# Optimization experiments

Measured on AMD Instinct MI355X. Metric: run time of the kernel, lower is better.

The kernel has to match this reference:

```python
import jax, jax.numpy as jnp
import numpy as np

B, N, D, H, FF = 2, 2048, 768, 12, 3072
HD = D // H
RADIUS = 2.0
COORD_DIM = 3
LN_EPS = 1e-5


def _layernorm(x, g, b):
    m = jnp.mean(x, axis=-1, keepdims=True)
    v = jnp.mean((x - m) ** 2, axis=-1, keepdims=True)
    return (x - m) * jax.lax.rsqrt(v + LN_EPS) * g + b


def setup_inputs() -> dict:
    key = jax.random.key(0)
    ks = jax.random.split(key, 16)
    s = 0.02
    return {
        "x": jax.random.normal(ks[0], (B, N, D), jnp.float32),
        "coords": jax.random.uniform(ks[1], (B, N, COORD_DIM), jnp.float32) * 10.0,
        "w_qkv": jax.random.normal(ks[2], (D, 3 * D), jnp.float32) * s,
        "b_qkv": jnp.zeros((3 * D,), jnp.float32),
        "w_out": jax.random.normal(ks[3], (D, D), jnp.float32) * s,
        "b_out": jnp.zeros((D,), jnp.float32),
        "w_ff1": jax.random.normal(ks[4], (D, FF), jnp.float32) * s,
        "b_ff1": jnp.zeros((FF,), jnp.float32),
        "w_ff2": jax.random.normal(ks[5], (FF, D), jnp.float32) * s,
        "b_ff2": jnp.zeros((D,), jnp.float32),
        "g1": jnp.ones((D,), jnp.float32),
        "beta1": jnp.zeros((D,), jnp.float32),
        "g2": jnp.ones((D,), jnp.float32),
        "beta2": jnp.zeros((D,), jnp.float32),
    }


def reference(x, coords, w_qkv, b_qkv, w_out, b_out, w_ff1, b_ff1,
              w_ff2, b_ff2, g1, beta1, g2, beta2):
    # --- attention sub-block ---
    residual = x
    xn = _layernorm(x, g1, beta1)
    qkv = xn @ w_qkv + b_qkv                       # [B,N,3D]
    qkv = qkv.reshape(B, N, 3, H, HD)
    q, k, v = qkv[:, :, 0], qkv[:, :, 1], qkv[:, :, 2]   # [B,N,H,HD]

    # geometric radius mask: attend only to tokens within Euclidean RADIUS
    d2 = jnp.sum((coords[:, :, None, :] - coords[:, None, :, :]) ** 2, axis=-1)  # [B,N,N]
    mask = d2 <= RADIUS * RADIUS                   # self-distance 0 -> always true

    scores = jnp.einsum("bqhd,bkhd->bhqk", q, k) / jnp.sqrt(jnp.float32(HD))
    scores = jnp.where(mask[:, None, :, :], scores, jnp.float32(-1e9))
    attn = jax.nn.softmax(scores, axis=-1)
    attn_out = jnp.einsum("bhqk,bkhd->bqhd", attn, v).reshape(B, N, D)
    attn_out = attn_out @ w_out + b_out            # dropout=0 (eval)
    x = residual + attn_out

    # --- FFN sub-block ---
    residual = x
    xn = _layernorm(x, g2, beta2)
    h = jax.nn.gelu(xn @ w_ff1 + b_ff1, approximate=False)
    ff_out = h @ w_ff2 + b_ff2
    return residual + ff_out
```

## Files before the change

### kernel.cpp

```cpp
#include <hip/hip_runtime.h>
#include <hip/hip_bf16.h>

typedef unsigned short ushort_t;
typedef __attribute__((ext_vector_type(4))) float f32x4;
typedef __attribute__((ext_vector_type(8))) short s16x8;

#define DEV static __device__ __forceinline__

constexpr int Bb = 2, Nn = 2048, Dd = 768, Hh = 12, FFf = 3072;
constexpr int MTOK = Bb * Nn;
constexpr int QKVN = 3 * Dd;

DEV unsigned short f2bf(float f) {
    union { float f; unsigned int i; } x; x.f = f;
    unsigned int r = x.i + 0x7FFFu + ((x.i >> 16) & 1u);
    return (unsigned short)(r >> 16);
}

DEV void gload16(const void* g, void* l) {
    __builtin_amdgcn_global_load_lds(
        (const __attribute__((address_space(1))) void*)g,
        (__attribute__((address_space(3))) void*)l, 16, 0, 0);
}

DEV int xcd_swz(int lin, int n) {
    return (lin & 7) * (n >> 3) + (lin >> 3);
}

__global__ void k_transpose(const float* __restrict__ in, unsigned short* __restrict__ out,
                            int K, int N) {
    __shared__ float t[32][33];
    int bx = blockIdx.x * 32, by = blockIdx.y * 32;
    int tx = threadIdx.x, ty = threadIdx.y;
#pragma unroll
    for (int i = 0; i < 4; i++)
        t[ty + 8 * i][tx] = in[(size_t)(by + ty + 8 * i) * N + bx + tx];
    __syncthreads();
#pragma unroll
    for (int i = 0; i < 4; i++)
        out[(size_t)(bx + ty + 8 * i) * K + by + tx] = f2bf(t[tx][ty + 8 * i]);
}

__global__ void k_coords(const float* __restrict__ c, float4* __restrict__ out, int n) {
    int i = blockIdx.x * 256 + threadIdx.x;
    if (i < n) out[i] = make_float4(c[3 * i], c[3 * i + 1], c[3 * i + 2], 0.f);
}

DEV int cell_of(float4 c) {
    int cx = (int)(c.x * 0.5f); cx = cx > 4 ? 4 : cx;
    int cy = (int)(c.y * 0.5f); cy = cy > 4 ? 4 : cy;
    int cz = (int)(c.z * 0.5f); cz = cz > 4 ? 4 : cz;
    return (cz * 5 + cy) * 5 + cx;
}

__global__ __launch_bounds__(256) void k_sort(const float4* __restrict__ c4,
                                              int* __restrict__ s2o,
                                              float4* __restrict__ c4s) {
    int b = blockIdx.y;
    int i = blockIdx.x * 4 + (threadIdx.x >> 6);
    int lane = threadIdx.x & 63;
    const float4* cb = c4 + b * Nn;
    float4 ci = cb[i];
    int celli = cell_of(ci);
    int pos = 0;
    for (int it = 0; it < Nn / 64; it++) {
        int j = it * 64 + lane;
        int cj = cell_of(cb[j]);
        bool before = (cj < celli) || (cj == celli && j < i);
        pos += __popcll(__ballot(before));
    }
    if (lane == 0) {
        s2o[b * Nn + pos] = i;
        c4s[b * Nn + pos] = ci;
    }
}

__global__ __launch_bounds__(256) void k_mask(const float4* __restrict__ c4s,
                                              unsigned long long* __restrict__ mb) {
    int qt = blockIdx.x, ks = blockIdx.y, b = blockIdx.z;
    __shared__ float4 ck[256];
    int t = threadIdx.x;
    ck[t] = c4s[b * Nn + ks * 256 + t];
    __syncthreads();
    int r = t >> 2, c = t & 3;
    int q = qt * 64 + r;
    float4 cq = c4s[b * Nn + q];
    unsigned long long w = 0;
#pragma unroll 8
    for (int j = 0; j < 64; j++) {
        float4 k4 = ck[c * 64 + j];
        float dx = __fsub_rn(cq.x, k4.x);
        float dy = __fsub_rn(cq.y, k4.y);
        float dz = __fsub_rn(cq.z, k4.z);
        float d2 = __fadd_rn(__fadd_rn(__fmul_rn(dx, dx), __fmul_rn(dy, dy)),
                             __fmul_rn(dz, dz));
        if (d2 <= 4.0f) w |= 1ull << j;
    }
    mb[((size_t)(b * Nn + q) << 5) + ks * 4 + c] = w;
}

__global__ __launch_bounds__(64) void k_tiles(const unsigned long long* __restrict__ mb,
                                              int* __restrict__ tl) {
    int q64 = blockIdx.x, b = blockIdx.y;
    int lane = threadIdx.x;
    unsigned long long v = 0;
    if (lane < 32) {
        const unsigned long long* base = mb + ((size_t)(b * Nn + q64 * 64) << 5) + lane;
        for (int r = 0; r < 64; r++) v |= base[(size_t)r << 5];
    }
    unsigned long long nz = __ballot(v != 0);
    int idx = __popcll(nz & ((1ull << lane) - 1));
    int* o = tl + (b * 32 + q64) * 33;
    if (v != 0) o[1 + idx] = lane;
    if (lane == 0) o[0] = __popcll(nz);
}

__global__ __launch_bounds__(128) void k_gatherK(const unsigned short* __restrict__ qkv,
                                                 const int* __restrict__ s2o,
                                                 unsigned short* __restrict__ Ksort) {
    int ns = blockIdx.x & (Nn - 1);
    int b = blockIdx.x >> 11;
    int t = threadIdx.x;
    int orig = s2o[b * Nn + ns];
    const s16x8* src = (const s16x8*)(qkv + ((size_t)b * Nn + orig) * QKVN + Dd);
    s16x8* dst = (s16x8*)(Ksort + ((size_t)b * Nn + ns) * Dd);
    if (t < 96) dst[t] = src[t];
}

__global__ __launch_bounds__(256) void k_vt(const unsigned short* __restrict__ qkv,
                                            const int* __restrict__ s2o,
                                            unsigned short* __restrict__ VtT) {
    __shared__ unsigned short Ld[64][72];
    int ns0 = blockIdx.x * 64;
    int bh = blockIdx.y;
    int b = bh / Hh, h = bh % Hh;
    int t = threadIdx.x;
#pragma unroll
    for (int i = 0; i < 2; i++) {
        int item = t + 256 * i;
        int row = item >> 3, ch = (item & 7) * 8;
        int orig = s2o[b * Nn + ns0 + row];
        *(s16x8*)&Ld[row][ch] =
            *(const s16x8*)(qkv + ((size_t)b * Nn + orig) * QKVN + 2 * Dd + h * 64 + ch);
    }
    __syncthreads();
    int vd = (t >> 5) * 8, vkp = (t & 31) * 2;
#pragma unroll
    for (int j = 0; j < 8; j++) {
        unsigned int pack = (unsigned int)Ld[vkp][vd + j] |
                            ((unsigned int)Ld[vkp + 1][vd + j] << 16);
        *(unsigned int*)((char*)VtT +
                         (((size_t)bh * 64 + vd + j) * Nn + ns0 + vkp) * 2) = pack;
    }
}

DEV float wred_sum(float v) {
#pragma unroll
    for (int o = 32; o; o >>= 1) v += __shfl_down(v, o, 64);
    return v;
}

__global__ __launch_bounds__(256) void k_ln(const float* __restrict__ x,
                                            const float* __restrict__ g,
                                            const float* __restrict__ be,
                                            unsigned short* __restrict__ out) {
    int row = blockIdx.x;
    const float* xr = x + (size_t)row * Dd;
    int t = threadIdx.x;
    float v0 = xr[t], v1 = xr[t + 256], v2 = xr[t + 512];
    float s = v0 + v1 + v2;
    float sq = v0 * v0 + v1 * v1 + v2 * v2;
    __shared__ float r1[4], r2[4];
    float ws = wred_sum(s), wq = wred_sum(sq);
    int wid = t >> 6, lane = t & 63;
    if (lane == 0) { r1[wid] = ws; r2[wid] = wq; }
    __syncthreads();
    s = r1[0] + r1[1] + r1[2] + r1[3];
    sq = r2[0] + r2[1] + r2[2] + r2[3];
    float mean = s * (1.f / Dd);
    float var = sq * (1.f / Dd) - mean * mean;
    float rs = rsqrtf(var + 1e-5f);
    unsigned short* orow = out + (size_t)row * Dd;
    orow[t]       = f2bf((v0 - mean) * rs * g[t]       + be[t]);
    orow[t + 256] = f2bf((v1 - mean) * rs * g[t + 256] + be[t + 256]);
    orow[t + 512] = f2bf((v2 - mean) * rs * g[t + 512] + be[t + 512]);
}

template <int EPI>
__global__ __launch_bounds__(256) void k_gemm(const unsigned short* __restrict__ A,
                                              const unsigned short* __restrict__ Bt,
                                              const float* __restrict__ bias,
                                              const float* __restrict__ res,
                                              void* __restrict__ outp,
                                              int M, int N, int K) {
    constexpr int BM = 128, BN = 128, BK = 32;
    __shared__ unsigned short As[BM][BK];
    __shared__ unsigned short Bs[BN][BK];
    int NB = N >> 7;
    int id = xcd_swz(blockIdx.x, gridDim.x);
    int m0 = (id / NB) * BM, n0 = (id % NB) * BN;
    int t = threadIdx.x;
    int wid = t >> 6, lane = t & 63;
    int wr = wid >> 1, wc = wid & 1;
    int lg = lane >> 4, lr = lane & 15;
    f32x4 acc[4][4] = {};

    int srow = wid * 32 + (lane >> 2);
    int scol = (lane & 3) * 8;
    const unsigned short* Ag = A + (size_t)(m0 + srow) * K + scol;
    const unsigned short* Bg = Bt + (size_t)(n0 + srow) * K + scol;
    char* Al = (char*)&As[0][0] + wid * 2048;
    char* Bl = (char*)&Bs[0][0] + wid * 2048;

    for (int k0 = 0; k0 < K; k0 += BK) {
        __syncthreads();
        gload16(Ag + k0, Al);
        gload16(Ag + k0 + (size_t)16 * K, Al + 1024);
        gload16(Bg + k0, Bl);
        gload16(Bg + k0 + (size_t)16 * K, Bl + 1024);
        __syncthreads();
        s16x8 af[4], bfr[4];
#pragma unroll
        for (int i = 0; i < 4; i++) {
            af[i]  = *(const s16x8*)&As[wr * 64 + i * 16 + lr][lg * 8];
            bfr[i] = *(const s16x8*)&Bs[wc * 64 + i * 16 + lr][lg * 8];
        }
#pragma unroll
        for (int mi = 0; mi < 4; mi++)
#pragma unroll
            for (int ni = 0; ni < 4; ni++)
                acc[mi][ni] = __builtin_amdgcn_mfma_f32_16x16x32_bf16(
                    af[mi], bfr[ni], acc[mi][ni], 0, 0, 0);
    }

    int mrow = m0 + wr * 64;
    int ncol = n0 + wc * 64;
#pragma unroll
    for (int mi = 0; mi < 4; mi++) {
#pragma unroll
        for (int ni = 0; ni < 4; ni++) {
            int nn = ncol + ni * 16 + lr;
            float bs = bias[nn];
#pragma unroll
            for (int r = 0; r < 4; r++) {
                int mm = mrow + mi * 16 + lg * 4 + r;
                float v = acc[mi][ni][r] + bs;
                if (EPI == 1) {
                    v = 0.5f * v * (1.f + erff(v * 0.70710678118f));
                    ((unsigned short*)outp)[(size_t)mm * N + nn] = f2bf(v);
                } else if (EPI == 2) {
                    v += res[(size_t)mm * N + nn];
                    ((float*)outp)[(size_t)mm * N + nn] = v;
                } else {
                    ((unsigned short*)outp)[(size_t)mm * N + nn] = f2bf(v);
                }
            }
        }
    }
}

template <int SPLIT>
__global__ __launch_bounds__(256) void k_gemm_sk(const unsigned short* __restrict__ A,
                                                 const unsigned short* __restrict__ Bt,
                                                 float* __restrict__ part,
                                                 int M, int N, int K) {
    constexpr int BM = 128, BN = 128, BK = 32;
    __shared__ unsigned short As[BM][BK];
    __shared__ unsigned short Bs[BN][BK];
    int NB = N >> 7, MB = M >> 7;
    int id = xcd_swz(blockIdx.x, gridDim.x);
    int nb = id % NB;
    int mb = (id / NB) % MB;
    int kz = id / (NB * MB);
    int m0 = mb * BM, n0 = nb * BN;
    int Kc = K / SPLIT, kb = kz * Kc;
    int t = threadIdx.x;
    int wid = t >> 6, lane = t & 63;
    int wr = wid >> 1, wc = wid & 1;
    int lg = lane >> 4, lr = lane & 15;
    f32x4 acc[4][4] = {};

    int srow = wid * 32 + (lane >> 2);
    int scol = (lane & 3) * 8;
    const unsigned short* Ag = A + (size_t)(m0 + srow) * K + scol;
    const unsigned short* Bg = Bt + (size_t)(n0 + srow) * K + scol;
    char* Al = (char*)&As[0][0] + wid * 2048;
    char* Bl = (char*)&Bs[0][0] + wid * 2048;

    for (int k0 = kb; k0 < kb + Kc; k0 += BK) {
        __syncthreads();
        gload16(Ag + k0, Al);
        gload16(Ag + k0 + (size_t)16 * K, Al + 1024);
        gload16(Bg + k0, Bl);
        gload16(Bg + k0 + (size_t)16 * K, Bl + 1024);
        __syncthreads();
        s16x8 af[4], bfr[4];
#pragma unroll
        for (int i = 0; i < 4; i++) {
            af[i]  = *(const s16x8*)&As[wr * 64 + i * 16 + lr][lg * 8];
            bfr[i] = *(const s16x8*)&Bs[wc * 64 + i * 16 + lr][lg * 8];
        }
#pragma unroll
        for (int mi = 0; mi < 4; mi++)
#pragma unroll
            for (int ni = 0; ni < 4; ni++)
                acc[mi][ni] = __builtin_amdgcn_mfma_f32_16x16x32_bf16(
                    af[mi], bfr[ni], acc[mi][ni], 0, 0, 0);
    }

    float* po = part + (size_t)kz * M * N;
    int mrow = m0 + wr * 64;
    int ncol = n0 + wc * 64;
#pragma unroll
    for (int mi = 0; mi < 4; mi++)
#pragma unroll
        for (int ni = 0; ni < 4; ni++) {
            int nn = ncol + ni * 16 + lr;
#pragma unroll
            for (int r = 0; r < 4; r++) {
                int mm = mrow + mi * 16 + lg * 4 + r;
                po[(size_t)mm * N + nn] = acc[mi][ni][r];
            }
        }
}

__global__ __launch_bounds__(256) void k_reduce2(const float* __restrict__ part,
                                                 const float* __restrict__ bias,
                                                 const float* __restrict__ res,
                                                 float* __restrict__ out,
                                                 int MN, int N) {
    int i = (blockIdx.x * 256 + threadIdx.x) * 4;
    f32x4 a = *(const f32x4*)(part + i);
    f32x4 bq = *(const f32x4*)(part + (size_t)MN + i);
    f32x4 r = *(const f32x4*)(res + i);
    f32x4 bs = *(const f32x4*)(bias + (i % N));
    f32x4 o;
#pragma unroll
    for (int j = 0; j < 4; j++) o[j] = a[j] + bq[j] + bs[j] + r[j];
    *(f32x4*)(out + i) = o;
}

constexpr float SC2 = 0.125f * 1.44269504088896340736f;
constexpr float PMASK = -3.0e38f;
constexpr float MINIT = -1.0e30f;

__global__ __launch_bounds__(256) void k_attn(const unsigned short* __restrict__ qkv,
                                              const unsigned short* __restrict__ Ksort,
                                              const unsigned short* __restrict__ VtT,
                                              const int* __restrict__ s2o,
                                              const uint2* __restrict__ mb,
                                              const int* __restrict__ tl,
                                              unsigned short* __restrict__ out) {
    int lin = blockIdx.x;
    int id = (lin & 7) * 96 + (lin >> 3);
    int q64 = id & 31;
    int hb = id >> 5;
    int h = hb % Hh, b = hb / Hh;
    int bh = b * Hh + h;

    __shared__ __align__(16) char sm[2 * 16384 + 4 * 2048];

    int t = threadIdx.x, wid = t >> 6, lane = t & 63;
    int lg = lane >> 4, lr = lane & 15;
    int sw = lr & 7;
    int qbase = q64 * 64 + wid * 16;

    int oq = s2o[b * Nn + qbase + lr];
    const unsigned short* Qb = qkv + ((size_t)b * Nn + oq) * QKVN + h * 64;
    s16x8 qf0 = *(const s16x8*)(Qb + lg * 8);
    s16x8 qf1 = *(const s16x8*)(Qb + 32 + lg * 8);

    const uint2* mrow = mb + ((size_t)(b * Nn + qbase + lr) << 5);
    const int* tle = tl + (b * 32 + q64) * 33;
    int tlv = (lane < 33) ? tle[lane] : 0;
    int cnt = __shfl(tlv, 0, 64);

    int srow = lane >> 3, sch = lane & 7;
    int krow = wid * 8 + srow;
    int kx = sch ^ (krow & 7);
    const unsigned short* Kg0 = Ksort + ((size_t)b * Nn + krow) * Dd + h * 64 + kx * 8;
    const unsigned short* Vg0 = VtT + ((size_t)bh * 64 + krow) * Nn + kx * 8;
    char* pw = sm + 32768 + wid * 2048 + lr * 128;

    float m2 = MINIT, l_run = 0.f;
    f32x4 oacc[4] = {};

    int tid0 = __shfl(tlv, 1, 64);
    uint2 Mw = mrow[tid0];
    {
        char* Kl = sm + wid * 1024;
        gload16(Kg0 + (size_t)(tid0 * 64) * Dd, Kl);
        gload16(Kg0 + (size_t)(tid0 * 64 + 32) * Dd, Kl + 4096);
        char* Vl = sm + 8192 + wid * 1024;
        gload16(Vg0 + tid0 * 64, Vl);
        gload16(Vg0 + tid0 * 64 + 32 * (size_t)Nn, Vl + 4096);
    }
    __syncthreads();

    for (int ti = 0; ti < cnt; ti++) {
        int cur = ti & 1;
        uint2 MwN;
        if (ti + 1 < cnt) {
            int tidn = __shfl(tlv, 2 + ti, 64);
            char* Kl = sm + (cur ^ 1) * 16384 + wid * 1024;
            gload16(Kg0 + (size_t)(tidn * 64) * Dd, Kl);
            gload16(Kg0 + (size_t)(tidn * 64 + 32) * Dd, Kl + 4096);
            char* Vl = sm + (cur ^ 1) * 16384 + 8192 + wid * 1024;
            gload16(Vg0 + tidn * 64, Vl);
            gload16(Vg0 + tidn * 64 + 32 * (size_t)Nn, Vl + 4096);
            MwN = mrow[tidn];
        }

        if (__any((Mw.x | Mw.y) != 0)) {
            const char* Kbuf = sm + cur * 16384;
            const char* Vbuf = Kbuf + 8192;

            __builtin_amdgcn_s_setprio(1);
            f32x4 st[4];
#pragma unroll
            for (int s = 0; s < 4; s++) {
                const char* kr = Kbuf + (s * 16 + lr) * 128;
                s16x8 kf0 = *(const s16x8*)(kr + ((lg ^ sw) << 4));
                s16x8 kf1 = *(const s16x8*)(kr + (((4 + lg) ^ sw) << 4));
                f32x4 z = {};
                z = __builtin_amdgcn_mfma_f32_16x16x32_bf16(kf0, qf0, z, 0, 0, 0);
                st[s] = __builtin_amdgcn_mfma_f32_16x16x32_bf16(kf1, qf1, z, 0, 0, 0);
            }
            __builtin_amdgcn_s_setprio(0);

            float p[4][4];
            float mt = PMASK;
#pragma unroll
            for (int s = 0; s < 4; s++) {
                unsigned int wsel = (s < 2) ? Mw.x : Mw.y;
#pragma unroll
                for (int r = 0; r < 4; r++) {
                    float sv = st[s][r] * SC2;
                    unsigned int bit = (wsel >> ((s & 1) * 16 + lg * 4 + r)) & 1u;
                    p[s][r] = bit ? sv : PMASK;
                    mt = fmaxf(mt, p[s][r]);
                }
            }
            mt = fmaxf(mt, __shfl_xor(mt, 16, 64));
            mt = fmaxf(mt, __shfl_xor(mt, 32, 64));

            if (!__all(mt <= m2 + 11.5416f)) {
                float mn2 = fmaxf(m2, mt);
                float fac = __builtin_amdgcn_exp2f(m2 - mn2);
                l_run *= fac;
                m2 = mn2;
                float fr[4];
#pragma unroll
                for (int r = 0; r < 4; r++) fr[r] = __shfl(fac, (lane & 48) + lg * 4 + r, 64);
#pragma unroll
                for (int dt = 0; dt < 4; dt++)
#pragma unroll
                    for (int r = 0; r < 4; r++) oacc[dt][r] *= fr[r];
            }

            float lt = 0.f;
#pragma unroll
            for (int s = 0; s < 4; s++)
#pragma unroll
                for (int r = 0; r < 4; r++) {
                    p[s][r] = __builtin_amdgcn_exp2f(p[s][r] - m2);
                    lt += p[s][r];
                }
            lt += __shfl_xor(lt, 16, 64);
            lt += __shfl_xor(lt, 32, 64);
            l_run += lt;

#pragma unroll
            for (int s = 0; s < 4; s++) {
                unsigned int lo = (unsigned int)f2bf(p[s][0]) | ((unsigned int)f2bf(p[s][1]) << 16);
                unsigned int hi = (unsigned int)f2bf(p[s][2]) | ((unsigned int)f2bf(p[s][3]) << 16);
                unsigned long long u = (unsigned long long)lo | ((unsigned long long)hi << 32);
                int chunk = (s * 2 + (lg >> 1)) ^ sw;
                *(unsigned long long*)(pw + (chunk << 4) + (lg & 1) * 8) = u;
            }

            __builtin_amdgcn_s_setprio(1);
#pragma unroll
            for (int c = 0; c < 2; c++) {
                s16x8 pf = *(const s16x8*)(pw + (((c * 4 + lg) ^ sw) << 4));
#pragma unroll
                for (int dt = 0; dt < 4; dt++) {
                    const char* vr = Vbuf + (dt * 16 + lr) * 128;
                    s16x8 vf = *(const s16x8*)(vr + (((c * 4 + lg) ^ sw) << 4));
                    oacc[dt] = __builtin_amdgcn_mfma_f32_16x16x32_bf16(pf, vf, oacc[dt], 0, 0, 0);
                }
            }
            __builtin_amdgcn_s_setprio(0);
        }

        __syncthreads();
        Mw = MwN;
    }

    float lr4[4];
    int orow[4];
#pragma unroll
    for (int r = 0; r < 4; r++) {
        lr4[r] = __shfl(l_run, (lane & 48) + lg * 4 + r, 64);
        orow[r] = s2o[b * Nn + qbase + lg * 4 + r];
    }
#pragma unroll
    for (int dt = 0; dt < 4; dt++)
#pragma unroll
        for (int r = 0; r < 4; r++) {
            float v = oacc[dt][r] / lr4[r];
            out[((size_t)b * Nn + orow[r]) * Dd + h * 64 + dt * 16 + lr] = f2bf(v);
        }
}

extern "C" void kernel_launch(void* const* d_in, const int* in_sizes, int n_in,
                              void* d_out, int out_size, void* d_ws, size_t ws_size,
                              hipStream_t stream) {
    const float* x      = (const float*)d_in[0];
    const float* coords = (const float*)d_in[1];
    const float* w_qkv  = (const float*)d_in[2];
    const float* b_qkv  = (const float*)d_in[3];
    const float* w_out  = (const float*)d_in[4];
    const float* b_out  = (const float*)d_in[5];
    const float* w_ff1  = (const float*)d_in[6];
    const float* b_ff1  = (const float*)d_in[7];
    const float* w_ff2  = (const float*)d_in[8];
    const float* b_ff2  = (const float*)d_in[9];
    const float* g1     = (const float*)d_in[10];
    const float* beta1  = (const float*)d_in[11];
    const float* g2     = (const float*)d_in[12];
    const float* beta2  = (const float*)d_in[13];

    char* ws = (char*)d_ws;
    size_t off = 0;
    auto alloc = [&](size_t bytes) {
        char* p = ws + off;
        off += (bytes + 255) & ~(size_t)255;
        return p;
    };
    unsigned short* w_qkv_t = (unsigned short*)alloc((size_t)QKVN * Dd * 2);
    unsigned short* w_out_t = (unsigned short*)alloc((size_t)Dd * Dd * 2);
    unsigned short* w_ff1_t = (unsigned short*)alloc((size_t)FFf * Dd * 2);
    unsigned short* w_ff2_t = (unsigned short*)alloc((size_t)Dd * FFf * 2);
    float4*         c4      = (float4*)alloc((size_t)MTOK * 16);
    float4*         c4s     = (float4*)alloc((size_t)MTOK * 16);
    int*            s2o     = (int*)alloc((size_t)MTOK * 4);
    unsigned long long* mbits = (unsigned long long*)alloc((size_t)MTOK * 32 * 8);
    int*            tl      = (int*)alloc((size_t)Bb * 32 * 33 * 4);
    unsigned short* xn      = (unsigned short*)alloc((size_t)MTOK * Dd * 2);
    unsigned short* hbuf    = (unsigned short*)alloc((size_t)MTOK * FFf * 2);
    float*          x2      = (float*)alloc((size_t)MTOK * Dd * 4);
    unsigned short* attn_o  = (unsigned short*)alloc((size_t)MTOK * Dd * 2);
    unsigned short* qkv     = (unsigned short*)alloc((size_t)MTOK * QKVN * 2);
    unsigned short* Ksort   = (unsigned short*)alloc((size_t)MTOK * Dd * 2);
    unsigned short* VtT     = (unsigned short*)alloc((size_t)Bb * Hh * 64 * Nn * 2);
    float* partial = (float*)qkv;

    dim3 tb(32, 8);
    k_transpose<<<dim3(QKVN / 32, Dd / 32), tb, 0, stream>>>(w_qkv, w_qkv_t, Dd, QKVN);
    k_transpose<<<dim3(Dd / 32, Dd / 32), tb, 0, stream>>>(w_out, w_out_t, Dd, Dd);
    k_transpose<<<dim3(FFf / 32, Dd / 32), tb, 0, stream>>>(w_ff1, w_ff1_t, Dd, FFf);
    k_transpose<<<dim3(Dd / 32, FFf / 32), tb, 0, stream>>>(w_ff2, w_ff2_t, FFf, Dd);
    k_coords<<<(MTOK + 255) / 256, 256, 0, stream>>>(coords, c4, MTOK);
    k_sort<<<dim3(Nn / 4, Bb), 256, 0, stream>>>(c4, s2o, c4s);
    k_mask<<<dim3(Nn / 64, 8, Bb), 256, 0, stream>>>(c4s, mbits);
    k_tiles<<<dim3(32, Bb), 64, 0, stream>>>(mbits, tl);

    k_ln<<<MTOK, 256, 0, stream>>>(x, g1, beta1, xn);
    k_gemm<0><<<dim3((QKVN / 128) * (MTOK / 128)), 256, 0, stream>>>(
        xn, w_qkv_t, b_qkv, nullptr, qkv, MTOK, QKVN, Dd);
    k_gatherK<<<dim3(MTOK), 128, 0, stream>>>(qkv, s2o, Ksort);
    k_vt<<<dim3(Nn / 64, Bb * Hh), 256, 0, stream>>>(qkv, s2o, VtT);
    k_attn<<<dim3((Nn / 64) * Hh * Bb), 256, 0, stream>>>(
        qkv, Ksort, VtT, s2o, (const uint2*)mbits, tl, attn_o);
    k_gemm<2><<<dim3((Dd / 128) * (MTOK / 128)), 256, 0, stream>>>(
        attn_o, w_out_t, b_out, x, x2, MTOK, Dd, Dd);
    k_ln<<<MTOK, 256, 0, stream>>>(x2, g2, beta2, xn);
    k_gemm<1><<<dim3((FFf / 128) * (MTOK / 128)), 256, 0, stream>>>(
        xn, w_ff1_t, b_ff1, nullptr, hbuf, MTOK, FFf, Dd);
    k_gemm_sk<2><<<dim3((Dd / 128) * (MTOK / 128) * 2), 256, 0, stream>>>(
        hbuf, w_ff2_t, partial, MTOK, Dd, FFf);
    k_reduce2<<<dim3(MTOK * Dd / 1024), 256, 0, stream>>>(
        partial, b_ff2, x2, (float*)d_out, MTOK * Dd, Dd);
}
```

Measured before the change: 227.3 us.

## Double-buffer GEMM LDS tiles and split-K the attention output projection

Both GEMM kernels now keep two LDS buffers and load the next K tile asynchronously while MFMAs run on the current one. Waits use explicit vmcnt counts and raw s_barrier, with setprio raised around the MFMA block. The attention output projection switches from the fused-residual GEMM to the split-K GEMM plus a reduce kernel, so the small 768x768 problem launches more blocks. This adds an extra launch and a round trip of partial sums through memory, and the hand-written waitcnt logic must exactly match the four global loads issued per stage.

Measured after the change: 220.5 us. 3.0% less time.

```diff
diff --git a/kernel.cpp b/kernel.cpp
--- a/kernel.cpp
+++ b/kernel.cpp
@@ -186,6 +186,37 @@
     orow[t + 512] = f2bf((v2 - mean) * rs * g[t + 512] + be[t + 512]);
 }
 
+#define GEMM_PIPE_LOOP(NT)                                                              \
+    stage(0, 0);                                                                        \
+    for (int t = 0; t < (NT); t++) {                                                    \
+        int cur = t & 1;                                                                \
+        if (t + 1 < (NT)) {                                                             \
+            stage(cur ^ 1, t + 1);                                                      \
+            asm volatile("s_waitcnt vmcnt(4)" ::: "memory");                            \
+        } else {                                                                        \
+            asm volatile("s_waitcnt vmcnt(0)" ::: "memory");                            \
+        }                                                                               \
+        __builtin_amdgcn_sched_barrier(0);                                              \
+        __builtin_amdgcn_s_barrier();                                                   \
+        const unsigned short* Ab = As[cur];                                             \
+        const unsigned short* Bbp = Bs[cur];                                            \
+        s16x8 af[4], bfr[4];                                                            \
+        _Pragma("unroll")                                                               \
+        for (int i = 0; i < 4; i++) {                                                   \
+            af[i]  = *(const s16x8*)&Ab[(wr * 64 + i * 16 + lr) * 32 + lg * 8];         \
+            bfr[i] = *(const s16x8*)&Bbp[(wc * 64 + i * 16 + lr) * 32 + lg * 8];        \
+        }                                                                               \
+        __builtin_amdgcn_s_setprio(1);                                                  \
+        _Pragma("unroll")                                                               \
+        for (int mi = 0; mi < 4; mi++)                                                  \
+            _Pragma("unroll")                                                           \
+            for (int ni = 0; ni < 4; ni++)                                              \
+                acc[mi][ni] = __builtin_amdgcn_mfma_f32_16x16x32_bf16(                  \
+                    af[mi], bfr[ni], acc[mi][ni], 0, 0, 0);                             \
+        __builtin_amdgcn_s_setprio(0);                                                  \
+        __builtin_amdgcn_s_barrier();                                                   \
+    }
+
 template <int EPI>
 __global__ __launch_bounds__(256) void k_gemm(const unsigned short* __restrict__ A,
                                               const unsigned short* __restrict__ Bt,
@@ -194,8 +225,8 @@
                                               void* __restrict__ outp,
                                               int M, int N, int K) {
     constexpr int BM = 128, BN = 128, BK = 32;
-    __shared__ unsigned short As[BM][BK];
-    __shared__ unsigned short Bs[BN][BK];
+    __shared__ unsigned short As[2][BM * BK];
+    __shared__ unsigned short Bs[2][BN * BK];
     int NB = N >> 7;
     int id = xcd_swz(blockIdx.x, gridDim.x);
     int m0 = (id / NB) * BM, n0 = (id % NB) * BN;
@@ -209,29 +240,18 @@
     int scol = (lane & 3) * 8;
     const unsigned short* Ag = A + (size_t)(m0 + srow) * K + scol;
     const unsigned short* Bg = Bt + (size_t)(n0 + srow) * K + scol;
-    char* Al = (char*)&As[0][0] + wid * 2048;
-    char* Bl = (char*)&Bs[0][0] + wid * 2048;
-
-    for (int k0 = 0; k0 < K; k0 += BK) {
-        __syncthreads();
+
+    auto stage = [&](int buf, int kt) {
+        int k0 = kt * BK;
+        char* Al = (char*)As[buf] + wid * 2048;
+        char* Bl = (char*)Bs[buf] + wid * 2048;
         gload16(Ag + k0, Al);
         gload16(Ag + k0 + (size_t)16 * K, Al + 1024);
         gload16(Bg + k0, Bl);
         gload16(Bg + k0 + (size_t)16 * K, Bl + 1024);
-        __syncthreads();
-        s16x8 af[4], bfr[4];
-#pragma unroll
-        for (int i = 0; i < 4; i++) {
-            af[i]  = *(const s16x8*)&As[wr * 64 + i * 16 + lr][lg * 8];
-            bfr[i] = *(const s16x8*)&Bs[wc * 64 + i * 16 + lr][lg * 8];
-        }
-#pragma unroll
-        for (int mi = 0; mi < 4; mi++)
-#pragma unroll
-            for (int ni = 0; ni < 4; ni++)
-                acc[mi][ni] = __builtin_amdgcn_mfma_f32_16x16x32_bf16(
-                    af[mi], bfr[ni], acc[mi][ni], 0, 0, 0);
-    }
+    };
+    int nt = K / BK;
+    GEMM_PIPE_LOOP(nt)
 
     int mrow = m0 + wr * 64;
     int ncol = n0 + wc * 64;
@@ -265,15 +285,15 @@
                                                  float* __restrict__ part,
                                                  int M, int N, int K) {
     constexpr int BM = 128, BN = 128, BK = 32;
-    __shared__ unsigned short As[BM][BK];
-    __shared__ unsigned short Bs[BN][BK];
+    __shared__ unsigned short As[2][BM * BK];
+    __shared__ unsigned short Bs[2][BN * BK];
     int NB = N >> 7, MB = M >> 7;
     int id = xcd_swz(blockIdx.x, gridDim.x);
     int nb = id % NB;
-    int mb = (id / NB) % MB;
+    int mbk = (id / NB) % MB;
     int kz = id / (NB * MB);
-    int m0 = mb * BM, n0 = nb * BN;
-    int Kc = K / SPLIT, kb = kz * Kc;
+    int m0 = mbk * BM, n0 = nb * BN;
+    int Kc = K / SPLIT, kb = kz * (Kc / BK);
     int t = threadIdx.x;
     int wid = t >> 6, lane = t & 63;
     int wr = wid >> 1, wc = wid & 1;
@@ -284,29 +304,18 @@
     int scol = (lane & 3) * 8;
     const unsigned short* Ag = A + (size_t)(m0 + srow) * K + scol;
     const unsigned short* Bg = Bt + (size_t)(n0 + srow) * K + scol;
-    char* Al = (char*)&As[0][0] + wid * 2048;
-    char* Bl = (char*)&Bs[0][0] + wid * 2048;
-
-    for (int k0 = kb; k0 < kb + Kc; k0 += BK) {
-        __syncthreads();
+
+    auto stage = [&](int buf, int kt) {
+        int k0 = (kb + kt) * BK;
+        char* Al = (char*)As[buf] + wid * 2048;
+        char* Bl = (char*)Bs[buf] + wid * 2048;
         gload16(Ag + k0, Al);
         gload16(Ag + k0 + (size_t)16 * K, Al + 1024);
         gload16(Bg + k0, Bl);
         gload16(Bg + k0 + (size_t)16 * K, Bl + 1024);
-        __syncthreads();
-        s16x8 af[4], bfr[4];
-#pragma unroll
-        for (int i = 0; i < 4; i++) {
-            af[i]  = *(const s16x8*)&As[wr * 64 + i * 16 + lr][lg * 8];
-            bfr[i] = *(const s16x8*)&Bs[wc * 64 + i * 16 + lr][lg * 8];
-        }
-#pragma unroll
-        for (int mi = 0; mi < 4; mi++)
-#pragma unroll
-            for (int ni = 0; ni < 4; ni++)
-                acc[mi][ni] = __builtin_amdgcn_mfma_f32_16x16x32_bf16(
-                    af[mi], bfr[ni], acc[mi][ni], 0, 0, 0);
-    }
+    };
+    int nt = Kc / BK;
+    GEMM_PIPE_LOOP(nt)
 
     float* po = part + (size_t)kz * M * N;
     int mrow = m0 + wr * 64;
@@ -573,8 +582,10 @@
     k_vt<<<dim3(Nn / 64, Bb * Hh), 256, 0, stream>>>(qkv, s2o, VtT);
     k_attn<<<dim3((Nn / 64) * Hh * Bb), 256, 0, stream>>>(
         qkv, Ksort, VtT, s2o, (const uint2*)mbits, tl, attn_o);
-    k_gemm<2><<<dim3((Dd / 128) * (MTOK / 128)), 256, 0, stream>>>(
-        attn_o, w_out_t, b_out, x, x2, MTOK, Dd, Dd);
+    k_gemm_sk<2><<<dim3((Dd / 128) * (MTOK / 128) * 2), 256, 0, stream>>>(
+        attn_o, w_out_t, partial, MTOK, Dd, Dd);
+    k_reduce2<<<dim3(MTOK * Dd / 1024), 256, 0, stream>>>(
+        partial, b_out, x, x2, MTOK * Dd, Dd);
     k_ln<<<MTOK, 256, 0, stream>>>(x2, g2, beta2, xn);
     k_gemm<1><<<dim3((FFf / 128) * (MTOK / 128)), 256, 0, stream>>>(
         xn, w_ff1_t, b_ff1, nullptr, hbuf, MTOK, FFf, Dd);
```
